# Kernel optimization log

Measured on AMD Instinct MI355X. Metric: run time of the kernel, lower is better.

## Reference

```python
import jax, jax.numpy as jnp
import numpy as np
import math


def setup_inputs() -> dict:
    key = jax.random.key(0)
    k1, k2 = jax.random.split(key)
    B, CK, H, W = 4, 128, 64, 64
    Mk = jax.random.normal(k1, (B, CK, H, W), dtype=jnp.float32)
    Qk = jax.random.normal(k2, (B, CK, H, W), dtype=jnp.float32)
    return {"Mk": Mk, "Qk": Qk}


def reference(Mk, Qk):
    B, CK, H, W = Mk.shape
    N = H * W
    mk = Mk.reshape(B, CK, N)   # [B, CK, N_mem]
    qk = Qk.reshape(B, CK, N)   # [B, CK, N_query]
    # squared norm of each memory key: [B, N_mem, 1]
    a_sq = jnp.sum(mk * mk, axis=1)[:, :, None]
    # inner products: [B, N_mem, N_query]
    ab = jnp.einsum('bcm,bcq->bmq', mk, qk)
    affinity = (2.0 * ab - a_sq) / math.sqrt(CK)
    # softmax over memory positions (axis=1), matching F.softmax(dim=1)
    affinity = jax.nn.softmax(affinity, axis=1)
    return affinity
```

## Files before the change

### kernel.cpp

```cpp
#include <hip/hip_runtime.h>
#include <cstdint>

#define CKDIM 128
#define MDIM  4096
#define QDIM  4096
#define BATCH 4

typedef __attribute__((ext_vector_type(8))) _Float16 half8;
typedef __attribute__((ext_vector_type(4))) float    f32x4;

#if __has_builtin(__builtin_amdgcn_exp2f)
#define EXP2(x) __builtin_amdgcn_exp2f(x)
#else
#define EXP2(x) exp2f(x)
#endif

#define ALPHA 0.12753139626596757f
#define K2A   0.25506279253193514f

__device__ inline void gl_lds16(const void* g, void* l) {
    __builtin_amdgcn_global_load_lds(
        (const __attribute__((address_space(1))) unsigned*)g,
        (__attribute__((address_space(3))) unsigned*)l, 16, 0, 0);
}

__global__ void convert_kernel(const float* __restrict__ Mk, const float* __restrict__ Qk,
                               _Float16* __restrict__ At, _Float16* __restrict__ Bt,
                               float* __restrict__ cm, float* __restrict__ sums) {
    __shared__ _Float16 T[128 * 130];
    __shared__ float    asqp[16][128];
    const int blk = blockIdx.x;
    const int mat = blk >> 7;
    const int b   = (blk >> 5) & 3;
    const int t   = blk & 31;
    const float* src = (mat ? Qk : Mk) + (size_t)b * CKDIM * MDIM + t * 128;
    const int tid = threadIdx.x;
    const int kg  = tid >> 4;
    const int ng  = tid & 15;

    float sq[8] = {0.f, 0.f, 0.f, 0.f, 0.f, 0.f, 0.f, 0.f};
    #pragma unroll
    for (int it = 0; it < 8; ++it) {
        int k = it * 16 + kg;
        const float* g = src + (size_t)k * MDIM + ng * 8;
        float4 v0 = *(const float4*)g;
        float4 v1 = *(const float4*)(g + 4);
        _Float16* p = &T[k * 130 + ng * 8];
        p[0] = (_Float16)v0.x; p[1] = (_Float16)v0.y; p[2] = (_Float16)v0.z; p[3] = (_Float16)v0.w;
        p[4] = (_Float16)v1.x; p[5] = (_Float16)v1.y; p[6] = (_Float16)v1.z; p[7] = (_Float16)v1.w;
        if (mat == 0) {
            sq[0] += v0.x * v0.x; sq[1] += v0.y * v0.y;
            sq[2] += v0.z * v0.z; sq[3] += v0.w * v0.w;
            sq[4] += v1.x * v1.x; sq[5] += v1.y * v1.y;
            sq[6] += v1.z * v1.z; sq[7] += v1.w * v1.w;
        }
    }
    if (mat == 0) {
        #pragma unroll
        for (int j = 0; j < 8; ++j) asqp[kg][ng * 8 + j] = sq[j];
    } else {
        if (tid < 128) sums[(blk & 127) * 128 + tid] = 0.f;
    }
    __syncthreads();
    #pragma unroll
    for (int it = 0; it < 8; ++it) {
        int idx = it * 256 + tid;
        int cc  = idx >> 7;
        int n   = idx & 127;
        half8 o;
        #pragma unroll
        for (int j = 0; j < 8; ++j) o[j] = T[(cc * 8 + j) * 130 + n];
        if (mat == 0) {
            _Float16* dst = At + (size_t)b * (MDIM * CKDIM)
                          + (size_t)(t * 4 + (n >> 5)) * 4096 + cc * 256 + (n & 31) * 8;
            *(half8*)dst = o;
        } else {
            _Float16* dst = Bt + (size_t)b * (QDIM * CKDIM)
                          + (size_t)t * 16384 + cc * 1024 + n * 8;
            *(half8*)dst = o;
        }
    }
    if (mat == 0 && tid < 128) {
        float s = 0.f;
        #pragma unroll
        for (int g = 0; g < 16; ++g) s += asqp[g][tid];
        cm[b * MDIM + t * 128 + tid] = -ALPHA * s;
    }
}

template <int WRITE>
__global__ __launch_bounds__(256, 4) void gemm_pass(
        const _Float16* __restrict__ At, const _Float16* __restrict__ Bt,
        const float* __restrict__ cmArr, float* __restrict__ sums,
        float* __restrict__ out) {
    __shared__ __align__(16) char ldsA[2][8192];
    const int tid  = threadIdx.x;
    const int lane = tid & 63;
    const int wv   = tid >> 6;
    const int g4   = lane >> 4;
    const int i    = lane & 15;

    const int wg = blockIdx.x;
    const int id = ((wg & 7) << 7) | (wg >> 3);
    const int b  = id >> 8;
    const int qs = (id >> 3) & 31;
    const int ms = id & 7;
    const int q0 = qs << 7;
    const int m0 = ms << 9;

    const char* Ab = (const char*)At + ((size_t)(b * 128 + ms * 16) << 13);
    const char* Bb = (const char*)Bt + ((size_t)(b * 32 + qs) << 15);
    const int   cmb = (b << 12) + m0;

    half8 bq[2][4];
    #pragma unroll
    for (int nf = 0; nf < 2; ++nf)
        #pragma unroll
        for (int t = 0; t < 4; ++t)
            bq[nf][t] = *(const half8*)(Bb + (t * 4 + g4) * 2048
                                           + (wv * 32 + nf * 16 + i) * 16);

    float rs0, rs1;
    if (WRITE) {
        rs0 = 1.0f / sums[(b << 12) + q0 + wv * 32 + i];
        rs1 = 1.0f / sums[(b << 12) + q0 + wv * 32 + 16 + i];
    }

    {
        unsigned o0 = (unsigned)wv * 1024u;
        unsigned o1 = 4096u + (unsigned)wv * 1024u;
        gl_lds16(Ab + o0 + lane * 16, ldsA[0] + o0);
        gl_lds16(Ab + o1 + lane * 16, ldsA[0] + o1);
    }
    f32x4 cm0 = *(const f32x4*)&cmArr[cmb + g4 * 4];
    f32x4 cm1 = *(const f32x4*)&cmArr[cmb + 16 + g4 * 4];
    asm volatile("s_waitcnt vmcnt(0)" ::: "memory");
    __syncthreads();

    float cs0 = 0.f, cs1 = 0.f;

    #pragma unroll 1
    for (int mt = 0; mt < 16; ++mt) {
        const char* lA = ldsA[mt & 1];
        f32x4 cmn0, cmn1;
        if (mt + 1 < 16) {
            const char* Asrc = Ab + ((size_t)(mt + 1) << 13);
            char* dst = ldsA[(mt + 1) & 1];
            unsigned o0 = (unsigned)wv * 1024u;
            unsigned o1 = 4096u + (unsigned)wv * 1024u;
            gl_lds16(Asrc + o0 + lane * 16, dst + o0);
            gl_lds16(Asrc + o1 + lane * 16, dst + o1);
            cmn0 = *(const f32x4*)&cmArr[cmb + (mt + 1) * 32 + g4 * 4];
            cmn1 = *(const f32x4*)&cmArr[cmb + (mt + 1) * 32 + 16 + g4 * 4];
        }
        __builtin_amdgcn_sched_barrier(0);

        f32x4 acc[2][2] = {};
        #pragma unroll
        for (int t = 0; t < 4; ++t) {
            const char* base = lA + (t * 4 + g4) * 512 + i * 16;
            half8 a0 = *(const half8*)(base);
            half8 a1 = *(const half8*)(base + 256);
            __builtin_amdgcn_s_setprio(1);
            acc[0][0] = __builtin_amdgcn_mfma_f32_16x16x32_f16(a0, bq[0][t], acc[0][0], 0, 0, 0);
            acc[0][1] = __builtin_amdgcn_mfma_f32_16x16x32_f16(a0, bq[1][t], acc[0][1], 0, 0, 0);
            acc[1][0] = __builtin_amdgcn_mfma_f32_16x16x32_f16(a1, bq[0][t], acc[1][0], 0, 0, 0);
            acc[1][1] = __builtin_amdgcn_mfma_f32_16x16x32_f16(a1, bq[1][t], acc[1][1], 0, 0, 0);
            __builtin_amdgcn_s_setprio(0);
        }

        if (WRITE) {
            #pragma unroll
            for (int mf = 0; mf < 2; ++mf) {
                f32x4  cmv  = mf ? cm1 : cm0;
                size_t mrow = (size_t)(m0 + mt * 32 + mf * 16 + g4 * 4);
                size_t base = ((((size_t)b << 12) + mrow) << 12) + (q0 + wv * 32 + i);
                #pragma unroll
                for (int r = 0; r < 4; ++r) {
                    out[base + ((size_t)r << 12)]      = EXP2(fmaf(acc[mf][0][r], K2A, cmv[r])) * rs0;
                    out[base + ((size_t)r << 12) + 16] = EXP2(fmaf(acc[mf][1][r], K2A, cmv[r])) * rs1;
                }
            }
        } else {
            #pragma unroll
            for (int mf = 0; mf < 2; ++mf) {
                f32x4 cmv = mf ? cm1 : cm0;
                #pragma unroll
                for (int r = 0; r < 4; ++r) {
                    cs0 += EXP2(fmaf(acc[mf][0][r], K2A, cmv[r]));
                    cs1 += EXP2(fmaf(acc[mf][1][r], K2A, cmv[r]));
                }
            }
        }

        if (mt + 1 < 16) {
            if (WRITE) asm volatile("s_waitcnt vmcnt(18)" ::: "memory");
            else       asm volatile("s_waitcnt vmcnt(2)"  ::: "memory");
            __builtin_amdgcn_s_barrier();
            __builtin_amdgcn_sched_barrier(0);
        }
        cm0 = cmn0; cm1 = cmn1;
    }

    if (!WRITE) {
        cs0 += __shfl_xor(cs0, 16); cs0 += __shfl_xor(cs0, 32);
        cs1 += __shfl_xor(cs1, 16); cs1 += __shfl_xor(cs1, 32);
        if (lane < 16) {
            __hip_atomic_fetch_add(&sums[(b << 12) + q0 + wv * 32 + lane], cs0,
                                   __ATOMIC_RELAXED, __HIP_MEMORY_SCOPE_AGENT);
            __hip_atomic_fetch_add(&sums[(b << 12) + q0 + wv * 32 + 16 + lane], cs1,
                                   __ATOMIC_RELAXED, __HIP_MEMORY_SCOPE_AGENT);
        }
    }
}

extern "C" void kernel_launch(void* const* d_in, const int* in_sizes, int n_in,
                              void* d_out, int out_size, void* d_ws, size_t ws_size,
                              hipStream_t stream) {
    const float* Mk = (const float*)d_in[0];
    const float* Qk = (const float*)d_in[1];
    float* out = (float*)d_out;

    _Float16* At   = (_Float16*)d_ws;
    _Float16* Bt   = At + (size_t)BATCH * MDIM * CKDIM;
    float*    sums = (float*)(Bt + (size_t)BATCH * MDIM * CKDIM);
    float*    cm   = sums + BATCH * QDIM;

    convert_kernel<<<256, 256, 0, stream>>>(Mk, Qk, At, Bt, cm, sums);
    gemm_pass<0><<<1024, 256, 0, stream>>>(At, Bt, cm, sums, out);
    gemm_pass<1><<<1024, 256, 0, stream>>>(At, Bt, cm, sums, out);
}
```

Measured before the change: 95.50 us.

## Switch to 32x32x16 MFMA with 2x2 wave tiling and 64-row M tiles

The GEMM passes move from 16x16x32 MFMA with four waves split along Q to 32x32x16 MFMA with waves arranged 2x2 over M and Q. Each iteration now covers 64 memory rows, which halves the number of loop iterations and barriers, and the A staging layout and LDS buffer are doubled to match. The convert kernel writes A in the new 64-row blocked layout. The cm values are now loaded inside the epilogue rather than prefetched, which may expose some load latency. The hand-tuned vmcnt counts were also changed and have to stay correct for the new number of outstanding loads and stores.

```diff
diff --git a/kernel.cpp b/kernel.cpp
--- a/kernel.cpp
+++ b/kernel.cpp
@@ -6,8 +6,9 @@
 #define QDIM  4096
 #define BATCH 4
 
-typedef __attribute__((ext_vector_type(8))) _Float16 half8;
-typedef __attribute__((ext_vector_type(4))) float    f32x4;
+typedef __attribute__((ext_vector_type(8)))  _Float16 half8;
+typedef __attribute__((ext_vector_type(4)))  float    f32x4;
+typedef __attribute__((ext_vector_type(16))) float    f32x16;
 
 #if __has_builtin(__builtin_amdgcn_exp2f)
 #define EXP2(x) __builtin_amdgcn_exp2f(x)
@@ -72,7 +73,7 @@
         for (int j = 0; j < 8; ++j) o[j] = T[(cc * 8 + j) * 130 + n];
         if (mat == 0) {
             _Float16* dst = At + (size_t)b * (MDIM * CKDIM)
-                          + (size_t)(t * 4 + (n >> 5)) * 4096 + cc * 256 + (n & 31) * 8;
+                          + (size_t)(t * 2 + (n >> 6)) * 8192 + cc * 512 + (n & 63) * 8;
             *(half8*)dst = o;
         } else {
             _Float16* dst = Bt + (size_t)b * (QDIM * CKDIM)
@@ -93,12 +94,14 @@
         const _Float16* __restrict__ At, const _Float16* __restrict__ Bt,
         const float* __restrict__ cmArr, float* __restrict__ sums,
         float* __restrict__ out) {
-    __shared__ __align__(16) char ldsA[2][8192];
+    __shared__ __align__(16) char ldsA[2][16384];
     const int tid  = threadIdx.x;
     const int lane = tid & 63;
     const int wv   = tid >> 6;
-    const int g4   = lane >> 4;
-    const int i    = lane & 15;
+    const int mg   = wv >> 1;
+    const int qg   = wv & 1;
+    const int l5   = lane >> 5;
+    const int l31  = lane & 31;
 
     const int wg = blockIdx.x;
     const int id = ((wg & 7) << 7) | (wg >> 3);
@@ -108,107 +111,97 @@
     const int q0 = qs << 7;
     const int m0 = ms << 9;
 
-    const char* Ab = (const char*)At + ((size_t)(b * 128 + ms * 16) << 13);
+    const char* Ab = (const char*)At + ((size_t)(b * 64 + ms * 8) << 14);
     const char* Bb = (const char*)Bt + ((size_t)(b * 32 + qs) << 15);
-    const int   cmb = (b << 12) + m0;
-
-    half8 bq[2][4];
-    #pragma unroll
-    for (int nf = 0; nf < 2; ++nf)
-        #pragma unroll
-        for (int t = 0; t < 4; ++t)
-            bq[nf][t] = *(const half8*)(Bb + (t * 4 + g4) * 2048
-                                           + (wv * 32 + nf * 16 + i) * 16);
+
+    half8 bq0[8], bq1[8];
+    #pragma unroll
+    for (int s = 0; s < 8; ++s) {
+        const char* p = Bb + (size_t)(2 * s + l5) * 2048 + (qg * 64 + l31) * 16;
+        bq0[s] = *(const half8*)(p);
+        bq1[s] = *(const half8*)(p + 512);
+    }
 
     float rs0, rs1;
     if (WRITE) {
-        rs0 = 1.0f / sums[(b << 12) + q0 + wv * 32 + i];
-        rs1 = 1.0f / sums[(b << 12) + q0 + wv * 32 + 16 + i];
-    }
-
-    {
-        unsigned o0 = (unsigned)wv * 1024u;
-        unsigned o1 = 4096u + (unsigned)wv * 1024u;
-        gl_lds16(Ab + o0 + lane * 16, ldsA[0] + o0);
-        gl_lds16(Ab + o1 + lane * 16, ldsA[0] + o1);
-    }
-    f32x4 cm0 = *(const f32x4*)&cmArr[cmb + g4 * 4];
-    f32x4 cm1 = *(const f32x4*)&cmArr[cmb + 16 + g4 * 4];
+        rs0 = 1.0f / sums[(b << 12) + q0 + qg * 64 + l31];
+        rs1 = 1.0f / sums[(b << 12) + q0 + qg * 64 + 32 + l31];
+    }
+
+    #pragma unroll
+    for (int r = 0; r < 4; ++r) {
+        unsigned Dw = r * 4096u + wv * 1024u;
+        gl_lds16(Ab + Dw + lane * 16, ldsA[0] + Dw);
+    }
     asm volatile("s_waitcnt vmcnt(0)" ::: "memory");
     __syncthreads();
 
+    const int cmbase = (b << 12) + m0 + mg * 32 + l5 * 4;
     float cs0 = 0.f, cs1 = 0.f;
 
     #pragma unroll 1
-    for (int mt = 0; mt < 16; ++mt) {
+    for (int mt = 0; mt < 8; ++mt) {
         const char* lA = ldsA[mt & 1];
-        f32x4 cmn0, cmn1;
-        if (mt + 1 < 16) {
-            const char* Asrc = Ab + ((size_t)(mt + 1) << 13);
+        if (mt + 1 < 8) {
+            const char* Asrc = Ab + ((size_t)(mt + 1) << 14);
             char* dst = ldsA[(mt + 1) & 1];
-            unsigned o0 = (unsigned)wv * 1024u;
-            unsigned o1 = 4096u + (unsigned)wv * 1024u;
-            gl_lds16(Asrc + o0 + lane * 16, dst + o0);
-            gl_lds16(Asrc + o1 + lane * 16, dst + o1);
-            cmn0 = *(const f32x4*)&cmArr[cmb + (mt + 1) * 32 + g4 * 4];
-            cmn1 = *(const f32x4*)&cmArr[cmb + (mt + 1) * 32 + 16 + g4 * 4];
+            #pragma unroll
+            for (int r = 0; r < 4; ++r) {
+                unsigned Dw = r * 4096u + wv * 1024u;
+                gl_lds16(Asrc + Dw + lane * 16, dst + Dw);
+            }
         }
         __builtin_amdgcn_sched_barrier(0);
 
-        f32x4 acc[2][2] = {};
-        #pragma unroll
-        for (int t = 0; t < 4; ++t) {
-            const char* base = lA + (t * 4 + g4) * 512 + i * 16;
-            half8 a0 = *(const half8*)(base);
-            half8 a1 = *(const half8*)(base + 256);
+        f32x16 acc0 = {}, acc1 = {};
+        #pragma unroll
+        for (int s = 0; s < 8; ++s) {
+            half8 a = *(const half8*)(lA + (2 * s + l5) * 1024 + (mg * 32 + l31) * 16);
             __builtin_amdgcn_s_setprio(1);
-            acc[0][0] = __builtin_amdgcn_mfma_f32_16x16x32_f16(a0, bq[0][t], acc[0][0], 0, 0, 0);
-            acc[0][1] = __builtin_amdgcn_mfma_f32_16x16x32_f16(a0, bq[1][t], acc[0][1], 0, 0, 0);
-            acc[1][0] = __builtin_amdgcn_mfma_f32_16x16x32_f16(a1, bq[0][t], acc[1][0], 0, 0, 0);
-            acc[1][1] = __builtin_amdgcn_mfma_f32_16x16x32_f16(a1, bq[1][t], acc[1][1], 0, 0, 0);
+            acc0 = __builtin_amdgcn_mfma_f32_32x32x16_f16(a, bq0[s], acc0, 0, 0, 0);
+            acc1 = __builtin_amdgcn_mfma_f32_32x32x16_f16(a, bq1[s], acc1, 0, 0, 0);
             __builtin_amdgcn_s_setprio(0);
         }
 
         if (WRITE) {
             #pragma unroll
-            for (int mf = 0; mf < 2; ++mf) {
-                f32x4  cmv  = mf ? cm1 : cm0;
-                size_t mrow = (size_t)(m0 + mt * 32 + mf * 16 + g4 * 4);
-                size_t base = ((((size_t)b << 12) + mrow) << 12) + (q0 + wv * 32 + i);
+            for (int j = 0; j < 4; ++j) {
+                f32x4 cmj = *(const f32x4*)&cmArr[cmbase + mt * 64 + j * 8];
                 #pragma unroll
-                for (int r = 0; r < 4; ++r) {
-                    out[base + ((size_t)r << 12)]      = EXP2(fmaf(acc[mf][0][r], K2A, cmv[r])) * rs0;
-                    out[base + ((size_t)r << 12) + 16] = EXP2(fmaf(acc[mf][1][r], K2A, cmv[r])) * rs1;
+                for (int rr = 0; rr < 4; ++rr) {
+                    int    row  = m0 + mt * 64 + mg * 32 + j * 8 + rr + l5 * 4;
+                    size_t base = ((((size_t)b << 12) + row) << 12) + q0 + qg * 64 + l31;
+                    out[base]      = EXP2(fmaf(acc0[j * 4 + rr], K2A, cmj[rr])) * rs0;
+                    out[base + 32] = EXP2(fmaf(acc1[j * 4 + rr], K2A, cmj[rr])) * rs1;
                 }
             }
         } else {
             #pragma unroll
-            for (int mf = 0; mf < 2; ++mf) {
-                f32x4 cmv = mf ? cm1 : cm0;
+            for (int j = 0; j < 4; ++j) {
+                f32x4 cmj = *(const f32x4*)&cmArr[cmbase + mt * 64 + j * 8];
                 #pragma unroll
-                for (int r = 0; r < 4; ++r) {
-                    cs0 += EXP2(fmaf(acc[mf][0][r], K2A, cmv[r]));
-                    cs1 += EXP2(fmaf(acc[mf][1][r], K2A, cmv[r]));
+                for (int rr = 0; rr < 4; ++rr) {
+                    cs0 += EXP2(fmaf(acc0[j * 4 + rr], K2A, cmj[rr]));
+                    cs1 += EXP2(fmaf(acc1[j * 4 + rr], K2A, cmj[rr]));
                 }
             }
         }
 
-        if (mt + 1 < 16) {
-            if (WRITE) asm volatile("s_waitcnt vmcnt(18)" ::: "memory");
-            else       asm volatile("s_waitcnt vmcnt(2)"  ::: "memory");
+        if (mt + 1 < 8) {
+            if (WRITE) asm volatile("s_waitcnt vmcnt(36)" ::: "memory");
+            else       asm volatile("s_waitcnt vmcnt(4)"  ::: "memory");
             __builtin_amdgcn_s_barrier();
             __builtin_amdgcn_sched_barrier(0);
         }
-        cm0 = cmn0; cm1 = cmn1;
     }
 
     if (!WRITE) {
-        cs0 += __shfl_xor(cs0, 16); cs0 += __shfl_xor(cs0, 32);
-        cs1 += __shfl_xor(cs1, 16); cs1 += __shfl_xor(cs1, 32);
-        if (lane < 16) {
-            __hip_atomic_fetch_add(&sums[(b << 12) + q0 + wv * 32 + lane], cs0,
+        cs0 += __shfl_xor(cs0, 32);
+        cs1 += __shfl_xor(cs1, 32);
+        if (lane < 32) {
+            __hip_atomic_fetch_add(&sums[(b << 12) + q0 + qg * 64 + lane], cs0,
                                    __ATOMIC_RELAXED, __HIP_MEMORY_SCOPE_AGENT);
-            __hip_atomic_fetch_add(&sums[(b << 12) + q0 + wv * 32 + 16 + lane], cs1,
+            __hip_atomic_fetch_add(&sums[(b << 12) + q0 + qg * 64 + 32 + lane], cs1,
                                    __ATOMIC_RELAXED, __HIP_MEMORY_SCOPE_AGENT);
         }
     }
```

Result: faster. 84.98 us (median of 2 runs) (-11.0%).
